# Kernel tuning notes

Hardware: AMD Instinct MI355X
Metric: run time of the kernel (lower is better)

Reference implementation:

```python
import jax, jax.numpy as jnp
import numpy as np

N = 100000      # nodes
E = 1600000     # edges (avg degree 16)
IN, HID, OUT = 128, 128, 64


def setup_inputs() -> dict:
    key = jax.random.key(0)
    k1, k2, k3, k4 = jax.random.split(key, 4)
    x = jax.random.normal(k1, (N, IN), dtype=jnp.float32)
    edge_index = jax.random.randint(k2, (2, E), 0, N, dtype=jnp.int64)
    # GCNConv linear weights (glorot-ish scale) and zero biases
    W1 = jax.random.normal(k3, (IN, HID), dtype=jnp.float32) * (1.0 / np.sqrt(IN))
    b1 = jnp.zeros((HID,), jnp.float32)
    W2 = jax.random.normal(k4, (HID, OUT), dtype=jnp.float32) * (1.0 / np.sqrt(HID))
    b2 = jnp.zeros((OUT,), jnp.float32)
    return {"x": x, "edge_index": edge_index, "W1": W1, "b1": b1, "W2": W2, "b2": b2}


def reference(x, edge_index, W1, b1, W2, b2):
    n = x.shape[0]
    loops = jnp.arange(n, dtype=edge_index.dtype)
    self_e = jnp.stack([loops, loops])  # [2, N]
    # forward() explicitly adds self-loops, then PyG GCNConv's gcn_norm
    # (add_self_loops=True by default) adds a second set -> duplicate (i,i) edges.
    ei = jnp.concatenate([edge_index, self_e, self_e], axis=1)
    row, col = ei[0], ei[1]  # source, target

    # symmetric normalization: deg over target index, norm_e = d^-1/2[row]*d^-1/2[col]
    deg = jax.ops.segment_sum(jnp.ones(row.shape, x.dtype), col, num_segments=n)
    dis = jax.lax.rsqrt(deg)  # deg >= 2 thanks to self-loops
    norm = dis[row] * dis[col]  # [E']

    def gcn_conv(h, W, b):
        h = h @ W                               # transform first (PyG order)
        msg = h[row] * norm[:, None]            # gather + per-edge scale
        agg = jax.ops.segment_sum(msg, col, num_segments=n)  # scatter-add
        return agg + b

    h = jax.nn.relu(gcn_conv(x, W1, b1))
    return gcn_conv(h, W2, b2)
```

## Files before the change

### kernel.cpp

```cpp
#include <hip/hip_runtime.h>
#include <hip/hip_fp16.h>

#define NPB   512
#define NBMAX 256
#define CHUNK 2048

using f16x4 = __attribute__((ext_vector_type(4))) _Float16;
using f32x4 = __attribute__((ext_vector_type(4))) float;

__global__ void k_detect(const int* __restrict__ ei32, int* __restrict__ flag,
                         int* __restrict__ bcnt, int nb) {
  int t = threadIdx.x;
  if (t < nb) bcnt[t] = 0;
  if (t == 0) {
    int z = 1;
    for (int k = 0; k < 64; ++k)
      if (ei32[2 * k + 1] != 0) { z = 0; break; }
    flag[0] = z;
  }
}

__device__ __forceinline__ int edge_at(const void* ei, int is64, long long pos) {
  return is64 ? (int)((const long long*)ei)[pos] : ((const int*)ei)[pos];
}

__global__ __launch_bounds__(256) void k_bcount(const void* __restrict__ ei,
                                                const int* __restrict__ flag,
                                                int E, int* __restrict__ bcnt, int nb) {
  __shared__ int cnt[NBMAX];
  int t = threadIdx.x;
  cnt[t] = 0;
  __syncthreads();
  int is64 = flag[0];
  int stride = gridDim.x * blockDim.x;
  for (int e = blockIdx.x * blockDim.x + t; e < E; e += stride) {
    int c = edge_at(ei, is64, (long long)E + e);
    atomicAdd(&cnt[c >> 9], 1);
  }
  __syncthreads();
  if (t < nb && cnt[t]) atomicAdd(&bcnt[t], cnt[t]);
}

__global__ void k_bscan(const int* __restrict__ bcnt, int* __restrict__ bbase,
                        int* __restrict__ bcur, int* __restrict__ rowptr,
                        int nb, int N, int E) {
  __shared__ int sh[NBMAX];
  int t = threadIdx.x;
  sh[t] = (t < nb) ? bcnt[t] : 0;
  __syncthreads();
  for (int off = 1; off < NBMAX; off <<= 1) {
    int x = 0;
    if (t >= off) x = sh[t - off];
    __syncthreads();
    if (t >= off) sh[t] += x;
    __syncthreads();
  }
  int excl = t ? sh[t - 1] : 0;
  if (t < nb) { bbase[t] = excl; bcur[t] = excl; }
  if (t == 0) { bbase[nb] = E; rowptr[N] = E; }
}

__global__ __launch_bounds__(256) void k_fillB(const void* __restrict__ ei,
                                               const int* __restrict__ flag, int E,
                                               int* __restrict__ bcur,
                                               int* __restrict__ tmp, int nb) {
  __shared__ int cntL[NBMAX], startL[NBMAX], curL[NBMAX], gofs[NBMAX];
  __shared__ int sh[NBMAX];
  __shared__ int stage[CHUNK];
  __shared__ unsigned char sbkt[CHUNK];
  int t = threadIdx.x;
  int is64 = flag[0];
  for (long long base = (long long)blockIdx.x * CHUNK; base < E;
       base += (long long)gridDim.x * CHUNK) {
    int m = (int)min((long long)CHUNK, (long long)E - base);
    cntL[t] = 0;
    __syncthreads();
    for (int i = t; i < m; i += 256) {
      int c = edge_at(ei, is64, (long long)E + base + i);
      atomicAdd(&cntL[c >> 9], 1);
    }
    __syncthreads();
    sh[t] = cntL[t];
    __syncthreads();
    for (int off = 1; off < NBMAX; off <<= 1) {
      int x = 0;
      if (t >= off) x = sh[t - off];
      __syncthreads();
      if (t >= off) sh[t] += x;
      __syncthreads();
    }
    int excl = t ? sh[t - 1] : 0;
    startL[t] = excl;
    curL[t] = excl;
    if (t < nb && cntL[t] > 0) gofs[t] = atomicAdd(&bcur[t], cntL[t]);
    __syncthreads();
    for (int i = t; i < m; i += 256) {
      int r = edge_at(ei, is64, base + i);
      int c = edge_at(ei, is64, (long long)E + base + i);
      int b = c >> 9;
      int p = atomicAdd(&curL[b], 1);
      stage[p] = ((c & 511) << 17) | r;
      sbkt[p] = (unsigned char)b;
    }
    __syncthreads();
    for (int i = t; i < m; i += 256) {
      int b = sbkt[i];
      tmp[gofs[b] + (i - startL[b])] = stage[i];
    }
    __syncthreads();
  }
}

__global__ __launch_bounds__(256) void k_fillC(const int* __restrict__ tmp,
                                               const int* __restrict__ bbase,
                                               int* __restrict__ rowptr,
                                               float* __restrict__ dis,
                                               int* __restrict__ esrc, int N) {
  __shared__ int cnt[NPB];
  __shared__ int loc[NPB];
  __shared__ int sh[256];
  int b = blockIdx.x, t = threadIdx.x;
  int beg = bbase[b], end = bbase[b + 1];
  int base_node = b << 9;
  cnt[t] = 0; cnt[t + 256] = 0;
  __syncthreads();
  for (int e = beg + t; e < end; e += 256)
    atomicAdd(&cnt[tmp[e] >> 17], 1);
  __syncthreads();
  int c0 = cnt[2 * t], c1 = cnt[2 * t + 1];
  sh[t] = c0 + c1;
  __syncthreads();
  for (int off = 1; off < 256; off <<= 1) {
    int x = 0;
    if (t >= off) x = sh[t - off];
    __syncthreads();
    if (t >= off) sh[t] += x;
    __syncthreads();
  }
  int pre = t ? sh[t - 1] : 0;
  loc[2 * t] = beg + pre;
  loc[2 * t + 1] = beg + pre + c0;
  int v0 = base_node + 2 * t, v1 = v0 + 1;
  if (v0 < N) { rowptr[v0] = beg + pre;      dis[v0] = rsqrtf((float)(c0 + 2)); }
  if (v1 < N) { rowptr[v1] = beg + pre + c0; dis[v1] = rsqrtf((float)(c1 + 2)); }
  __syncthreads();
  for (int e = beg + t; e < end; e += 256) {
    int u = tmp[e];
    int pos = atomicAdd(&loc[u >> 17], 1);
    esrc[pos] = u & 0x1FFFF;
  }
}

template <int BN, bool AHALF>
__global__ __launch_bounds__(256) void k_gemm_mfma(const void* __restrict__ Av,
                                                   const float* __restrict__ W,
                                                   const float* __restrict__ dis,
                                                   __half* __restrict__ C,
                                                   int M, int tiles) {
  __shared__ _Float16 Wt[BN][136];
  __shared__ _Float16 At[64][136];
  __shared__ float disL[64];
  constexpr int NT = BN / 64;
  constexpr int CH = BN / 4;
  int t = threadIdx.x;
  int lane = t & 63, w = t >> 6;
  int lrow = lane & 15;
  int kq = (lane >> 4) * 4;
  int wcol0 = w * (BN / 4);

  for (int idx = t; idx < 128 * BN / 4; idx += 256) {
    int k = idx / CH, c4 = (idx % CH) * 4;
    float4 v = *(const float4*)&W[(size_t)k * BN + c4];
    Wt[c4 + 0][k] = (_Float16)v.x;
    Wt[c4 + 1][k] = (_Float16)v.y;
    Wt[c4 + 2][k] = (_Float16)v.z;
    Wt[c4 + 3][k] = (_Float16)v.w;
  }

  for (int tile = blockIdx.x; tile < tiles; tile += gridDim.x) {
    int row0 = tile * 64;
    __syncthreads();
#pragma unroll
    for (int i = 0; i < 8; ++i) {
      int idx = t + i * 256;
      int r = idx >> 5, c = (idx & 31) * 4;
      int gr = row0 + r;
      f16x4 hv = {0, 0, 0, 0};
      if (gr < M) {
        if constexpr (AHALF) {
          hv = *(const f16x4*)&((const _Float16*)Av)[(size_t)gr * 128 + c];
        } else {
          float4 v = *(const float4*)&((const float*)Av)[(size_t)gr * 128 + c];
          hv = f16x4{(_Float16)v.x, (_Float16)v.y, (_Float16)v.z, (_Float16)v.w};
        }
      }
      *(f16x4*)&At[r][c] = hv;
    }
    if (t < 64) {
      int gr = row0 + t;
      disL[t] = (gr < M) ? dis[gr] : 0.f;
    }
    __syncthreads();
    f32x4 acc[4][NT];
#pragma unroll
    for (int mt = 0; mt < 4; ++mt)
#pragma unroll
      for (int nt = 0; nt < NT; ++nt) acc[mt][nt] = f32x4{0.f, 0.f, 0.f, 0.f};
#pragma unroll
    for (int k0 = 0; k0 < 128; k0 += 16) {
      int kk = k0 + kq;
      f16x4 a[4], b[NT];
#pragma unroll
      for (int mt = 0; mt < 4; ++mt)
        a[mt] = *(const f16x4*)&At[mt * 16 + lrow][kk];
#pragma unroll
      for (int nt = 0; nt < NT; ++nt)
        b[nt] = *(const f16x4*)&Wt[wcol0 + nt * 16 + lrow][kk];
#pragma unroll
      for (int mt = 0; mt < 4; ++mt)
#pragma unroll
        for (int nt = 0; nt < NT; ++nt)
          acc[mt][nt] = __builtin_amdgcn_mfma_f32_16x16x16f16(a[mt], b[nt],
                                                              acc[mt][nt], 0, 0, 0);
    }
    __syncthreads();
#pragma unroll
    for (int mt = 0; mt < 4; ++mt)
#pragma unroll
      for (int nt = 0; nt < NT; ++nt) {
        int cc = wcol0 + nt * 16 + lrow;
        int rr = mt * 16 + kq;
#pragma unroll
        for (int reg = 0; reg < 4; ++reg)
          At[rr + reg][cc] = (_Float16)(acc[mt][nt][reg] * disL[rr + reg]);
      }
    __syncthreads();
#pragma unroll
    for (int i = 0; i < BN / 16; ++i) {
      int idx = t + i * 256;
      int r = idx / CH, c = (idx % CH) * 4;
      int gr = row0 + r;
      if (gr < M)
        *(f16x4*)&C[(size_t)gr * BN + c] = *(const f16x4*)&At[r][c];
    }
  }
}

#define ACC4(u)                                                         \
  { __half2 p;                                                          \
    p = *(__half2*)&(u).x; a0 += __low2float(p); a1 += __high2float(p); \
    p = *(__half2*)&(u).y; a2 += __low2float(p); a3 += __high2float(p); }

__global__ __launch_bounds__(256) void k_gather128(const __half* __restrict__ t,
    const float* __restrict__ bias, const int* __restrict__ rowptr,
    const int* __restrict__ esrc, const float* __restrict__ dis,
    __half* __restrict__ o, int n) {
  int gw = (int)((blockIdx.x * blockDim.x + threadIdx.x) >> 6);
  int lane = threadIdx.x & 63;
  int nw = (int)((gridDim.x * blockDim.x) >> 6);
  int half = lane >> 5;
  int f = (lane & 31) * 4;
  for (int v = gw; v < n; v += nw) {
    float a0 = 0.f, a1 = 0.f, a2 = 0.f, a3 = 0.f;
    int beg = rowptr[v], end = rowptr[v + 1];
    int e = beg + half;
    for (; e + 14 < end; e += 16) {
      int s0 = esrc[e],      s1 = esrc[e + 2],  s2 = esrc[e + 4],  s3 = esrc[e + 6];
      int s4 = esrc[e + 8],  s5 = esrc[e + 10], s6 = esrc[e + 12], s7 = esrc[e + 14];
      uint2 u0 = *(const uint2*)&t[(size_t)s0 * 128 + f];
      uint2 u1 = *(const uint2*)&t[(size_t)s1 * 128 + f];
      uint2 u2 = *(const uint2*)&t[(size_t)s2 * 128 + f];
      uint2 u3 = *(const uint2*)&t[(size_t)s3 * 128 + f];
      uint2 u4 = *(const uint2*)&t[(size_t)s4 * 128 + f];
      uint2 u5 = *(const uint2*)&t[(size_t)s5 * 128 + f];
      uint2 u6 = *(const uint2*)&t[(size_t)s6 * 128 + f];
      uint2 u7 = *(const uint2*)&t[(size_t)s7 * 128 + f];
      ACC4(u0) ACC4(u1) ACC4(u2) ACC4(u3)
      ACC4(u4) ACC4(u5) ACC4(u6) ACC4(u7)
    }
    for (; e + 6 < end; e += 8) {
      int s0 = esrc[e], s1 = esrc[e + 2], s2 = esrc[e + 4], s3 = esrc[e + 6];
      uint2 u0 = *(const uint2*)&t[(size_t)s0 * 128 + f];
      uint2 u1 = *(const uint2*)&t[(size_t)s1 * 128 + f];
      uint2 u2 = *(const uint2*)&t[(size_t)s2 * 128 + f];
      uint2 u3 = *(const uint2*)&t[(size_t)s3 * 128 + f];
      ACC4(u0) ACC4(u1) ACC4(u2) ACC4(u3)
    }
    for (; e < end; e += 2) {
      int s0 = esrc[e];
      uint2 u0 = *(const uint2*)&t[(size_t)s0 * 128 + f];
      ACC4(u0)
    }
    if (half == 0) {
      uint2 uv = *(const uint2*)&t[(size_t)v * 128 + f];
      __half2 p;
      p = *(__half2*)&uv.x; a0 = fmaf(2.f, __low2float(p), a0); a1 = fmaf(2.f, __high2float(p), a1);
      p = *(__half2*)&uv.y; a2 = fmaf(2.f, __low2float(p), a2); a3 = fmaf(2.f, __high2float(p), a3);
    }
    a0 += __shfl_xor(a0, 32); a1 += __shfl_xor(a1, 32);
    a2 += __shfl_xor(a2, 32); a3 += __shfl_xor(a3, 32);
    if (half == 0) {
      float dv = dis[v];
      a0 = fmaxf(fmaf(dv, a0, bias[f]),     0.f);
      a1 = fmaxf(fmaf(dv, a1, bias[f + 1]), 0.f);
      a2 = fmaxf(fmaf(dv, a2, bias[f + 2]), 0.f);
      a3 = fmaxf(fmaf(dv, a3, bias[f + 3]), 0.f);
      __half2 h0 = __floats2half2_rn(a0, a1), h1 = __floats2half2_rn(a2, a3);
      uint2 uu;
      uu.x = *(unsigned int*)&h0; uu.y = *(unsigned int*)&h1;
      *(uint2*)&o[(size_t)v * 128 + f] = uu;
    }
  }
}

__global__ __launch_bounds__(256) void k_gather64(const __half* __restrict__ t,
    const float* __restrict__ bias, const int* __restrict__ rowptr,
    const int* __restrict__ esrc, const float* __restrict__ dis,
    float* __restrict__ o, int n) {
  int gw = (int)((blockIdx.x * blockDim.x + threadIdx.x) >> 6);
  int lane = threadIdx.x & 63;
  int nw = (int)((gridDim.x * blockDim.x) >> 6);
  int sub = lane >> 4;
  int f = (lane & 15) * 4;
  for (int v = gw; v < n; v += nw) {
    float a0 = 0.f, a1 = 0.f, a2 = 0.f, a3 = 0.f;
    int beg = rowptr[v], end = rowptr[v + 1];
    int e = beg + sub;
    for (; e + 12 < end; e += 16) {
      int s0 = esrc[e], s1 = esrc[e + 4], s2 = esrc[e + 8], s3 = esrc[e + 12];
      uint2 u0 = *(const uint2*)&t[(size_t)s0 * 64 + f];
      uint2 u1 = *(const uint2*)&t[(size_t)s1 * 64 + f];
      uint2 u2 = *(const uint2*)&t[(size_t)s2 * 64 + f];
      uint2 u3 = *(const uint2*)&t[(size_t)s3 * 64 + f];
      ACC4(u0) ACC4(u1) ACC4(u2) ACC4(u3)
    }
    for (; e < end; e += 4) {
      int s0 = esrc[e];
      uint2 u0 = *(const uint2*)&t[(size_t)s0 * 64 + f];
      ACC4(u0)
    }
    if (sub == 0) {
      uint2 uv = *(const uint2*)&t[(size_t)v * 64 + f];
      __half2 p;
      p = *(__half2*)&uv.x; a0 = fmaf(2.f, __low2float(p), a0); a1 = fmaf(2.f, __high2float(p), a1);
      p = *(__half2*)&uv.y; a2 = fmaf(2.f, __low2float(p), a2); a3 = fmaf(2.f, __high2float(p), a3);
    }
    a0 += __shfl_xor(a0, 16); a0 += __shfl_xor(a0, 32);
    a1 += __shfl_xor(a1, 16); a1 += __shfl_xor(a1, 32);
    a2 += __shfl_xor(a2, 16); a2 += __shfl_xor(a2, 32);
    a3 += __shfl_xor(a3, 16); a3 += __shfl_xor(a3, 32);
    if (sub == 0) {
      float dv = dis[v];
      float4 r;
      r.x = fmaf(dv, a0, bias[f]);     r.y = fmaf(dv, a1, bias[f + 1]);
      r.z = fmaf(dv, a2, bias[f + 2]); r.w = fmaf(dv, a3, bias[f + 3]);
      *(float4*)&o[(size_t)v * 64 + f] = r;
    }
  }
}

extern "C" void kernel_launch(void* const* d_in, const int* in_sizes, int n_in,
                              void* d_out, int out_size, void* d_ws, size_t ws_size,
                              hipStream_t stream) {
  const float* x  = (const float*)d_in[0];
  const void*  ei = d_in[1];
  const float* W1 = (const float*)d_in[2];
  const float* b1 = (const float*)d_in[3];
  const float* W2 = (const float*)d_in[4];
  const float* b2 = (const float*)d_in[5];
  const int N = in_sizes[0] / 128;
  const int E = in_sizes[1] / 2;
  float* out = (float*)d_out;
  const int nb = (N + NPB - 1) / NPB;

  size_t off = 0;
  auto alloc = [&](size_t bytes) -> void* {
    void* p = (char*)d_ws + off;
    off += (bytes + 255) & ~(size_t)255;
    return p;
  };
  int*    flag   = (int*)alloc(4);
  int*    bcnt   = (int*)alloc(NBMAX * 4);
  int*    bbase  = (int*)alloc((NBMAX + 1) * 4);
  int*    bcur   = (int*)alloc(NBMAX * 4);
  int*    rowptr = (int*)alloc(((size_t)N + 1) * 4);
  float*  dis    = (float*)alloc((size_t)N * 4);
  int*    tmp    = (int*)alloc((size_t)E * 4);
  int*    esrc   = (int*)alloc((size_t)E * 4);
  __half* t1     = (__half*)alloc((size_t)N * 128 * 2);
  __half* z1     = (__half*)alloc((size_t)N * 128 * 2);
  __half* t2     = t1;

  int nchunks = (E + CHUNK - 1) / CHUNK;
  int tiles = (N + 63) / 64;

  k_detect<<<1, 256, 0, stream>>>((const int*)ei, flag, bcnt, nb);
  k_bcount<<<1024, 256, 0, stream>>>(ei, flag, E, bcnt, nb);
  k_bscan<<<1, 256, 0, stream>>>(bcnt, bbase, bcur, rowptr, nb, N, E);
  k_fillB<<<nchunks, 256, 0, stream>>>(ei, flag, E, bcur, tmp, nb);
  k_fillC<<<nb, 256, 0, stream>>>(tmp, bbase, rowptr, dis, esrc, N);

  k_gemm_mfma<128, false><<<min(tiles, 768), 256, 0, stream>>>(x, W1, dis, t1, N, tiles);
  k_gather128<<<2048, 256, 0, stream>>>(t1, b1, rowptr, esrc, dis, z1, N);
  k_gemm_mfma<64, true><<<min(tiles, 768), 256, 0, stream>>>(z1, W2, dis, t2, N, tiles);
  k_gather64<<<2048, 256, 0, stream>>>(t2, b2, rowptr, esrc, dis, out, N);
}
```

Baseline: 241.7 us.

## Fuse first GEMM with edge bucketing and drop the global count pass

The separate bucket-count and scan pass before bucket fill is removed. Buckets are now written into fixed-capacity slots (E/nb+4096 each), and the prefix scan runs afterwards on the final cursors. The first GEMM no longer needs dis, so it runs inside one mega-kernel alongside the bucket fill, with blocks split by parity, to overlap compute-bound and memory-bound work. Because t1 is no longer pre-scaled, the first gather loads dis[src] per edge, which adds extra gathered loads. The fixed capacity could overflow on skewed degree distributions.

```diff
diff --git a/kernel.cpp b/kernel.cpp
--- a/kernel.cpp
+++ b/kernel.cpp
@@ -9,9 +9,9 @@
 using f32x4 = __attribute__((ext_vector_type(4))) float;
 
 __global__ void k_detect(const int* __restrict__ ei32, int* __restrict__ flag,
-                         int* __restrict__ bcnt, int nb) {
+                         int* __restrict__ bcur, int nb, int cap) {
   int t = threadIdx.x;
-  if (t < nb) bcnt[t] = 0;
+  if (t < nb) bcur[t] = t * cap;
   if (t == 0) {
     int z = 1;
     for (int k = 0; k < 64; ++k)
@@ -24,54 +24,21 @@
   return is64 ? (int)((const long long*)ei)[pos] : ((const int*)ei)[pos];
 }
 
-__global__ __launch_bounds__(256) void k_bcount(const void* __restrict__ ei,
-                                                const int* __restrict__ flag,
-                                                int E, int* __restrict__ bcnt, int nb) {
-  __shared__ int cnt[NBMAX];
-  int t = threadIdx.x;
-  cnt[t] = 0;
-  __syncthreads();
-  int is64 = flag[0];
-  int stride = gridDim.x * blockDim.x;
-  for (int e = blockIdx.x * blockDim.x + t; e < E; e += stride) {
-    int c = edge_at(ei, is64, (long long)E + e);
-    atomicAdd(&cnt[c >> 9], 1);
-  }
-  __syncthreads();
-  if (t < nb && cnt[t]) atomicAdd(&bcnt[t], cnt[t]);
-}
-
-__global__ void k_bscan(const int* __restrict__ bcnt, int* __restrict__ bbase,
-                        int* __restrict__ bcur, int* __restrict__ rowptr,
-                        int nb, int N, int E) {
-  __shared__ int sh[NBMAX];
-  int t = threadIdx.x;
-  sh[t] = (t < nb) ? bcnt[t] : 0;
-  __syncthreads();
-  for (int off = 1; off < NBMAX; off <<= 1) {
-    int x = 0;
-    if (t >= off) x = sh[t - off];
-    __syncthreads();
-    if (t >= off) sh[t] += x;
-    __syncthreads();
-  }
-  int excl = t ? sh[t - 1] : 0;
-  if (t < nb) { bbase[t] = excl; bcur[t] = excl; }
-  if (t == 0) { bbase[nb] = E; rowptr[N] = E; }
-}
-
-__global__ __launch_bounds__(256) void k_fillB(const void* __restrict__ ei,
-                                               const int* __restrict__ flag, int E,
-                                               int* __restrict__ bcur,
-                                               int* __restrict__ tmp, int nb) {
-  __shared__ int cntL[NBMAX], startL[NBMAX], curL[NBMAX], gofs[NBMAX];
-  __shared__ int sh[NBMAX];
-  __shared__ int stage[CHUNK];
-  __shared__ unsigned char sbkt[CHUNK];
+__device__ void fillB_body(char* smem, const void* __restrict__ ei,
+                           const int* __restrict__ flag, int E,
+                           int* __restrict__ bcur, int* __restrict__ tmp,
+                           int nb, int bid, int nblk) {
+  int* cntL   = (int*)smem;
+  int* startL = cntL + NBMAX;
+  int* curL   = startL + NBMAX;
+  int* gofs   = curL + NBMAX;
+  int* sh     = gofs + NBMAX;
+  int* stage  = sh + NBMAX;
+  unsigned char* sbkt = (unsigned char*)(stage + CHUNK);
   int t = threadIdx.x;
   int is64 = flag[0];
-  for (long long base = (long long)blockIdx.x * CHUNK; base < E;
-       base += (long long)gridDim.x * CHUNK) {
+  for (long long base = (long long)bid * CHUNK; base < E;
+       base += (long long)nblk * CHUNK) {
     int m = (int)min((long long)CHUNK, (long long)E - base);
     cntL[t] = 0;
     __syncthreads();
@@ -111,55 +78,15 @@
   }
 }
 
-__global__ __launch_bounds__(256) void k_fillC(const int* __restrict__ tmp,
-                                               const int* __restrict__ bbase,
-                                               int* __restrict__ rowptr,
-                                               float* __restrict__ dis,
-                                               int* __restrict__ esrc, int N) {
-  __shared__ int cnt[NPB];
-  __shared__ int loc[NPB];
-  __shared__ int sh[256];
-  int b = blockIdx.x, t = threadIdx.x;
-  int beg = bbase[b], end = bbase[b + 1];
-  int base_node = b << 9;
-  cnt[t] = 0; cnt[t + 256] = 0;
-  __syncthreads();
-  for (int e = beg + t; e < end; e += 256)
-    atomicAdd(&cnt[tmp[e] >> 17], 1);
-  __syncthreads();
-  int c0 = cnt[2 * t], c1 = cnt[2 * t + 1];
-  sh[t] = c0 + c1;
-  __syncthreads();
-  for (int off = 1; off < 256; off <<= 1) {
-    int x = 0;
-    if (t >= off) x = sh[t - off];
-    __syncthreads();
-    if (t >= off) sh[t] += x;
-    __syncthreads();
-  }
-  int pre = t ? sh[t - 1] : 0;
-  loc[2 * t] = beg + pre;
-  loc[2 * t + 1] = beg + pre + c0;
-  int v0 = base_node + 2 * t, v1 = v0 + 1;
-  if (v0 < N) { rowptr[v0] = beg + pre;      dis[v0] = rsqrtf((float)(c0 + 2)); }
-  if (v1 < N) { rowptr[v1] = beg + pre + c0; dis[v1] = rsqrtf((float)(c1 + 2)); }
-  __syncthreads();
-  for (int e = beg + t; e < end; e += 256) {
-    int u = tmp[e];
-    int pos = atomicAdd(&loc[u >> 17], 1);
-    esrc[pos] = u & 0x1FFFF;
-  }
-}
-
-template <int BN, bool AHALF>
-__global__ __launch_bounds__(256) void k_gemm_mfma(const void* __restrict__ Av,
-                                                   const float* __restrict__ W,
-                                                   const float* __restrict__ dis,
-                                                   __half* __restrict__ C,
-                                                   int M, int tiles) {
-  __shared__ _Float16 Wt[BN][136];
-  __shared__ _Float16 At[64][136];
-  __shared__ float disL[64];
+template <int BN, bool AHALF, bool PRESCALE>
+__device__ void gemm_body(char* smem, const void* __restrict__ Av,
+                          const float* __restrict__ W,
+                          const float* __restrict__ dis,
+                          __half* __restrict__ C, int M, int tiles,
+                          int bid, int nblk) {
+  _Float16 (*Wt)[136] = (_Float16(*)[136])smem;
+  _Float16 (*At)[136] = (_Float16(*)[136])(smem + sizeof(_Float16) * BN * 136);
+  float* disL = (float*)(smem + sizeof(_Float16) * (BN + 64) * 136);
   constexpr int NT = BN / 64;
   constexpr int CH = BN / 4;
   int t = threadIdx.x;
@@ -177,7 +104,7 @@
     Wt[c4 + 3][k] = (_Float16)v.w;
   }
 
-  for (int tile = blockIdx.x; tile < tiles; tile += gridDim.x) {
+  for (int tile = bid; tile < tiles; tile += nblk) {
     int row0 = tile * 64;
     __syncthreads();
 #pragma unroll
@@ -196,9 +123,11 @@
       }
       *(f16x4*)&At[r][c] = hv;
     }
-    if (t < 64) {
-      int gr = row0 + t;
-      disL[t] = (gr < M) ? dis[gr] : 0.f;
+    if constexpr (PRESCALE) {
+      if (t < 64) {
+        int gr = row0 + t;
+        disL[t] = (gr < M) ? dis[gr] : 0.f;
+      }
     }
     __syncthreads();
     f32x4 acc[4][NT];
@@ -231,8 +160,11 @@
         int cc = wcol0 + nt * 16 + lrow;
         int rr = mt * 16 + kq;
 #pragma unroll
-        for (int reg = 0; reg < 4; ++reg)
-          At[rr + reg][cc] = (_Float16)(acc[mt][nt][reg] * disL[rr + reg]);
+        for (int reg = 0; reg < 4; ++reg) {
+          float val = acc[mt][nt][reg];
+          if constexpr (PRESCALE) val *= disL[rr + reg];
+          At[rr + reg][cc] = (_Float16)val;
+        }
       }
     __syncthreads();
 #pragma unroll
@@ -246,10 +178,94 @@
   }
 }
 
-#define ACC4(u)                                                         \
-  { __half2 p;                                                          \
-    p = *(__half2*)&(u).x; a0 += __low2float(p); a1 += __high2float(p); \
-    p = *(__half2*)&(u).y; a2 += __low2float(p); a3 += __high2float(p); }
+__global__ __launch_bounds__(256) void k_mega1(
+    const void* __restrict__ x, const float* __restrict__ W1,
+    __half* __restrict__ t1, int M, int tiles,
+    const void* __restrict__ ei, const int* __restrict__ flag, int E,
+    int* __restrict__ bcur, int* __restrict__ tmp, int nb) {
+  extern __shared__ char smem[];
+  if (blockIdx.x & 1)
+    fillB_body(smem, ei, flag, E, bcur, tmp, nb, blockIdx.x >> 1, gridDim.x >> 1);
+  else
+    gemm_body<128, false, false>(smem, x, W1, nullptr, t1, M, tiles,
+                                 blockIdx.x >> 1, gridDim.x >> 1);
+}
+
+__global__ __launch_bounds__(256) void k_gemm2(
+    const void* __restrict__ Av, const float* __restrict__ W,
+    const float* __restrict__ dis, __half* __restrict__ C, int M, int tiles) {
+  extern __shared__ char smem[];
+  gemm_body<64, true, true>(smem, Av, W, dis, C, M, tiles, blockIdx.x, gridDim.x);
+}
+
+__global__ void k_bscan(const int* __restrict__ bcur, int cap,
+                        int* __restrict__ bbase, int* __restrict__ rowptr,
+                        int nb, int N, int E) {
+  __shared__ int sh[NBMAX];
+  int t = threadIdx.x;
+  sh[t] = (t < nb) ? (bcur[t] - t * cap) : 0;
+  __syncthreads();
+  for (int off = 1; off < NBMAX; off <<= 1) {
+    int x = 0;
+    if (t >= off) x = sh[t - off];
+    __syncthreads();
+    if (t >= off) sh[t] += x;
+    __syncthreads();
+  }
+  int excl = t ? sh[t - 1] : 0;
+  if (t < nb) bbase[t] = excl;
+  if (t == 0) { bbase[nb] = E; rowptr[N] = E; }
+}
+
+__global__ __launch_bounds__(256) void k_fillC(const int* __restrict__ tmp,
+                                               const int* __restrict__ bcur,
+                                               const int* __restrict__ bbase,
+                                               int cap, int* __restrict__ rowptr,
+                                               float* __restrict__ dis,
+                                               int* __restrict__ esrc, int N) {
+  __shared__ int cnt[NPB];
+  __shared__ int loc[NPB];
+  __shared__ int sh[256];
+  int b = blockIdx.x, t = threadIdx.x;
+  int beg = b * cap;
+  int end = bcur[b];
+  int outb = bbase[b];
+  int base_node = b << 9;
+  cnt[t] = 0; cnt[t + 256] = 0;
+  __syncthreads();
+  for (int e = beg + t; e < end; e += 256)
+    atomicAdd(&cnt[tmp[e] >> 17], 1);
+  __syncthreads();
+  int c0 = cnt[2 * t], c1 = cnt[2 * t + 1];
+  sh[t] = c0 + c1;
+  __syncthreads();
+  for (int off = 1; off < 256; off <<= 1) {
+    int x = 0;
+    if (t >= off) x = sh[t - off];
+    __syncthreads();
+    if (t >= off) sh[t] += x;
+    __syncthreads();
+  }
+  int pre = t ? sh[t - 1] : 0;
+  loc[2 * t] = outb + pre;
+  loc[2 * t + 1] = outb + pre + c0;
+  int v0 = base_node + 2 * t, v1 = v0 + 1;
+  if (v0 < N) { rowptr[v0] = outb + pre;      dis[v0] = rsqrtf((float)(c0 + 2)); }
+  if (v1 < N) { rowptr[v1] = outb + pre + c0; dis[v1] = rsqrtf((float)(c1 + 2)); }
+  __syncthreads();
+  for (int e = beg + t; e < end; e += 256) {
+    int u = tmp[e];
+    int pos = atomicAdd(&loc[u >> 17], 1);
+    esrc[pos] = u & 0x1FFFF;
+  }
+}
+
+#define ACC4F(nn, u)                                                     \
+  { __half2 p;                                                           \
+    p = *(__half2*)&(u).x;                                               \
+    a0 = fmaf(nn, __low2float(p), a0); a1 = fmaf(nn, __high2float(p), a1); \
+    p = *(__half2*)&(u).y;                                               \
+    a2 = fmaf(nn, __low2float(p), a2); a3 = fmaf(nn, __high2float(p), a3); }
 
 __global__ __launch_bounds__(256) void k_gather128(const __half* __restrict__ t,
     const float* __restrict__ bias, const int* __restrict__ rowptr,
@@ -261,12 +277,15 @@
   int half = lane >> 5;
   int f = (lane & 31) * 4;
   for (int v = gw; v < n; v += nw) {
+    float dv = dis[v];
     float a0 = 0.f, a1 = 0.f, a2 = 0.f, a3 = 0.f;
     int beg = rowptr[v], end = rowptr[v + 1];
     int e = beg + half;
     for (; e + 14 < end; e += 16) {
       int s0 = esrc[e],      s1 = esrc[e + 2],  s2 = esrc[e + 4],  s3 = esrc[e + 6];
       int s4 = esrc[e + 8],  s5 = esrc[e + 10], s6 = esrc[e + 12], s7 = esrc[e + 14];
+      float d0 = dis[s0], d1 = dis[s1], d2 = dis[s2], d3 = dis[s3];
+      float d4 = dis[s4], d5 = dis[s5], d6 = dis[s6], d7 = dis[s7];
       uint2 u0 = *(const uint2*)&t[(size_t)s0 * 128 + f];
       uint2 u1 = *(const uint2*)&t[(size_t)s1 * 128 + f];
       uint2 u2 = *(const uint2*)&t[(size_t)s2 * 128 + f];
@@ -275,32 +294,32 @@
       uint2 u5 = *(const uint2*)&t[(size_t)s5 * 128 + f];
       uint2 u6 = *(const uint2*)&t[(size_t)s6 * 128 + f];
       uint2 u7 = *(const uint2*)&t[(size_t)s7 * 128 + f];
-      ACC4(u0) ACC4(u1) ACC4(u2) ACC4(u3)
-      ACC4(u4) ACC4(u5) ACC4(u6) ACC4(u7)
+      ACC4F(d0, u0) ACC4F(d1, u1) ACC4F(d2, u2) ACC4F(d3, u3)
+      ACC4F(d4, u4) ACC4F(d5, u5) ACC4F(d6, u6) ACC4F(d7, u7)
     }
     for (; e + 6 < end; e += 8) {
       int s0 = esrc[e], s1 = esrc[e + 2], s2 = esrc[e + 4], s3 = esrc[e + 6];
+      float d0 = dis[s0], d1 = dis[s1], d2 = dis[s2], d3 = dis[s3];
       uint2 u0 = *(const uint2*)&t[(size_t)s0 * 128 + f];
       uint2 u1 = *(const uint2*)&t[(size_t)s1 * 128 + f];
       uint2 u2 = *(const uint2*)&t[(size_t)s2 * 128 + f];
       uint2 u3 = *(const uint2*)&t[(size_t)s3 * 128 + f];
-      ACC4(u0) ACC4(u1) ACC4(u2) ACC4(u3)
+      ACC4F(d0, u0) ACC4F(d1, u1) ACC4F(d2, u2) ACC4F(d3, u3)
     }
     for (; e < end; e += 2) {
       int s0 = esrc[e];
+      float d0 = dis[s0];
       uint2 u0 = *(const uint2*)&t[(size_t)s0 * 128 + f];
-      ACC4(u0)
+      ACC4F(d0, u0)
     }
     if (half == 0) {
+      float sc = 2.f * dv;
       uint2 uv = *(const uint2*)&t[(size_t)v * 128 + f];
-      __half2 p;
-      p = *(__half2*)&uv.x; a0 = fmaf(2.f, __low2float(p), a0); a1 = fmaf(2.f, __high2float(p), a1);
-      p = *(__half2*)&uv.y; a2 = fmaf(2.f, __low2float(p), a2); a3 = fmaf(2.f, __high2float(p), a3);
+      ACC4F(sc, uv)
     }
     a0 += __shfl_xor(a0, 32); a1 += __shfl_xor(a1, 32);
     a2 += __shfl_xor(a2, 32); a3 += __shfl_xor(a3, 32);
     if (half == 0) {
-      float dv = dis[v];
       a0 = fmaxf(fmaf(dv, a0, bias[f]),     0.f);
       a1 = fmaxf(fmaf(dv, a1, bias[f + 1]), 0.f);
       a2 = fmaxf(fmaf(dv, a2, bias[f + 2]), 0.f);
@@ -312,6 +331,11 @@
     }
   }
 }
+
+#define ACC4(u)                                                         \
+  { __half2 p;                                                          \
+    p = *(__half2*)&(u).x; a0 += __low2float(p); a1 += __high2float(p); \
+    p = *(__half2*)&(u).y; a2 += __low2float(p); a3 += __high2float(p); }
 
 __global__ __launch_bounds__(256) void k_gather64(const __half* __restrict__ t,
     const float* __restrict__ bias, const int* __restrict__ rowptr,
@@ -371,7 +395,8 @@
   const int N = in_sizes[0] / 128;
   const int E = in_sizes[1] / 2;
   float* out = (float*)d_out;
-  const int nb = (N + NPB - 1) / NPB;
+  const int nb  = (N + NPB - 1) / NPB;
+  const int cap = E / nb + 4096;
 
   size_t off = 0;
   auto alloc = [&](size_t bytes) -> void* {
@@ -380,28 +405,27 @@
     return p;
   };
   int*    flag   = (int*)alloc(4);
-  int*    bcnt   = (int*)alloc(NBMAX * 4);
+  int*    bcur   = (int*)alloc(NBMAX * 4);
   int*    bbase  = (int*)alloc((NBMAX + 1) * 4);
-  int*    bcur   = (int*)alloc(NBMAX * 4);
   int*    rowptr = (int*)alloc(((size_t)N + 1) * 4);
   float*  dis    = (float*)alloc((size_t)N * 4);
-  int*    tmp    = (int*)alloc((size_t)E * 4);
+  int*    tmp    = (int*)alloc(((size_t)nb * cap + 16384) * 4);
   int*    esrc   = (int*)alloc((size_t)E * 4);
   __half* t1     = (__half*)alloc((size_t)N * 128 * 2);
   __half* z1     = (__half*)alloc((size_t)N * 128 * 2);
   __half* t2     = t1;
 
-  int nchunks = (E + CHUNK - 1) / CHUNK;
   int tiles = (N + 63) / 64;
-
-  k_detect<<<1, 256, 0, stream>>>((const int*)ei, flag, bcnt, nb);
-  k_bcount<<<1024, 256, 0, stream>>>(ei, flag, E, bcnt, nb);
-  k_bscan<<<1, 256, 0, stream>>>(bcnt, bbase, bcur, rowptr, nb, N, E);
-  k_fillB<<<nchunks, 256, 0, stream>>>(ei, flag, E, bcur, tmp, nb);
-  k_fillC<<<nb, 256, 0, stream>>>(tmp, bbase, rowptr, dis, esrc, N);
-
-  k_gemm_mfma<128, false><<<min(tiles, 768), 256, 0, stream>>>(x, W1, dis, t1, N, tiles);
+  const int smem_mega  = (128 + 64) * 136 * 2 + 256;
+  const int smem_gemm2 = (64 + 64) * 136 * 2 + 256;
+
+  k_detect<<<1, 256, 0, stream>>>((const int*)ei, flag, bcur, nb, cap);
+  k_mega1<<<1550, 256, smem_mega, stream>>>(x, W1, t1, N, tiles,
+                                            ei, flag, E, bcur, tmp, nb);
+  k_bscan<<<1, 256, 0, stream>>>(bcur, cap, bbase, rowptr, nb, N, E);
+  k_fillC<<<nb, 256, 0, stream>>>(tmp, bcur, bbase, cap, rowptr, dis, esrc, N);
+
   k_gather128<<<2048, 256, 0, stream>>>(t1, b1, rowptr, esrc, dis, z1, N);
-  k_gemm_mfma<64, true><<<min(tiles, 768), 256, 0, stream>>>(z1, W2, dis, t2, N, tiles);
+  k_gemm2<<<min(tiles, 768), 256, smem_gemm2, stream>>>(z1, W2, dis, t2, N, tiles);
   k_gather64<<<2048, 256, 0, stream>>>(t2, b2, rowptr, esrc, dis, out, N);
 }
```

New measurement: 243.8 us. Within noise of the previous version (+0.9%).
